# Optimization experiments

Hardware: AMD Instinct MI355X
Metric: run time of the kernel (lower is better)

Reference implementation:

```python
import jax, jax.numpy as jnp
import numpy as np

N, D, H, O, E = 4096, 1024, 4096, 1024, 8
TOP_K = 2

def setup_inputs() -> dict:
    key = jax.random.key(0)
    k = jax.random.split(key, 4)
    x  = jax.random.normal(k[0], (N, D), dtype=jnp.float32)
    Wg = jax.random.normal(k[1], (D, E), dtype=jnp.float32) * (1.0 / np.sqrt(D))
    W1 = jax.random.normal(k[2], (E, D, H), dtype=jnp.float32) * (1.0 / np.sqrt(D))
    b1 = jnp.zeros((E, H), dtype=jnp.float32)
    W2 = jax.random.normal(k[3], (E, H, O), dtype=jnp.float32) * (1.0 / np.sqrt(H))
    b2 = jnp.zeros((E, O), dtype=jnp.float32)
    return {"x": x, "Wg": Wg, "W1": W1, "b1": b1, "W2": W2, "b2": b2}

def reference(x, Wg, W1, b1, W2, b2):
    # Gate: Linear(bias=False) -> ReLU (lin() appends act) -> softmax
    logits = jax.nn.relu(x @ Wg)                      # [N, E]
    probs = jax.nn.softmax(logits, axis=1)            # [N, E]
    top_p, sel = jax.lax.top_k(probs, TOP_K)          # [N, K]
    top_p = top_p / jnp.sum(top_p, axis=-1, keepdims=True)
    # Per-token combine weights over experts: [N, E]
    combine = jnp.sum(jax.nn.one_hot(sel, E, dtype=x.dtype) * top_p[..., None], axis=1)
    # Experts: ReLU(x W1 + b1) -> ReLU(h W2 + b2); final ReLU because lin() adds act on output layer
    h = jax.nn.relu(jnp.einsum('nd,edh->enh', x, W1) + b1[:, None, :])   # [E, N, H]
    y = jax.nn.relu(jnp.einsum('enh,eho->eno', h, W2) + b2[:, None, :])  # [E, N, O]
    out = jnp.einsum('eno,ne->no', y, combine)                            # [N, O]
    return out
```

## Files before the change

### kernel.cpp

```cpp
#include <hip/hip_runtime.h>
#include <cstdint>

#define NTOK 4096
#define DDIM 1024
#define HDIM 4096
#define ODIM 1024
#define NEXP 8
#define NSLOT (2*NTOK)
#define MAXT128 72
#define MAXT256 40

typedef __bf16 bf16x8 __attribute__((ext_vector_type(8)));
typedef float  f32x4  __attribute__((ext_vector_type(4)));
typedef unsigned short ushort8v __attribute__((ext_vector_type(8)));

__device__ __forceinline__ unsigned short f2bf(float f) {
    union { float f; unsigned int u; } v; v.f = f;
    unsigned int r = (v.u + 0x7FFF + ((v.u >> 16) & 1)) >> 16;
    return (unsigned short)r;
}

typedef const void __attribute__((address_space(1)))* gas_ptr;
typedef void       __attribute__((address_space(3)))* las_ptr;

__global__ void gate_kernel(const float* __restrict__ x, const float* __restrict__ Wg,
                            int2* __restrict__ sel, float2* __restrict__ wts,
                            int* __restrict__ counts, unsigned short* __restrict__ xb) {
    int wave = threadIdx.x >> 6;
    int lane = threadIdx.x & 63;
    int n = blockIdx.x * 4 + wave;
    float acc[NEXP];
#pragma unroll
    for (int e = 0; e < NEXP; e++) acc[e] = 0.f;
    const float* xr = x + (size_t)n * DDIM;
    unsigned short* xbr = xb + (size_t)n * DDIM;
#pragma unroll
    for (int i = 0; i < 4; i++) {
        int d = i * 256 + lane * 4;
        float4 xv = *(const float4*)&xr[d];
        ushort4 o;
        o.x = f2bf(xv.x); o.y = f2bf(xv.y); o.z = f2bf(xv.z); o.w = f2bf(xv.w);
        *(ushort4*)&xbr[d] = o;
        const float* wr = Wg + (size_t)d * NEXP;
#pragma unroll
        for (int jj = 0; jj < 4; jj++) {
            float xs = (jj == 0) ? xv.x : (jj == 1) ? xv.y : (jj == 2) ? xv.z : xv.w;
#pragma unroll
            for (int e = 0; e < NEXP; e++)
                acc[e] = fmaf(xs, wr[jj * NEXP + e], acc[e]);
        }
    }
#pragma unroll
    for (int e = 0; e < NEXP; e++) {
#pragma unroll
        for (int off = 32; off >= 1; off >>= 1)
            acc[e] += __shfl_xor(acc[e], off, 64);
    }
    if (lane == 0) {
        float l0 = -1e30f, l1 = -1e30f; int e0 = 0, e1 = 0;
#pragma unroll
        for (int e = 0; e < NEXP; e++) {
            float v = fmaxf(acc[e], 0.f);
            if (v > l0)      { l1 = l0; e1 = e0; l0 = v; e0 = e; }
            else if (v > l1) { l1 = v;  e1 = e; }
        }
        float w0 = 1.f / (1.f + expf(l1 - l0));
        sel[n] = make_int2(e0, e1);
        wts[n] = make_float2(w0, 1.f - w0);
        atomicAdd(&counts[e0], 1);
        atomicAdd(&counts[e1], 1);
    }
}

__global__ void route_kernel(const int2* __restrict__ sel, const float2* __restrict__ wts,
                             const int* __restrict__ counts, int* __restrict__ offsets,
                             int4* __restrict__ t128, int* __restrict__ nt128,
                             int4* __restrict__ t256, int* __restrict__ nt256,
                             int* __restrict__ slot_token, float* __restrict__ slot_weight) {
    __shared__ int cur[NEXP];
    int t = threadIdx.x;
    if (t == 0) {
        int s = 0, n1 = 0, n2 = 0;
        for (int e = 0; e < NEXP; e++) {
            offsets[e] = s; cur[e] = s;
            int c = counts[e];
            for (int r = 0; r < c; r += 128)
                t128[n1++] = make_int4(e, s + r, min(128, c - r), 0);
            for (int r = 0; r < c; r += 256)
                t256[n2++] = make_int4(e, s + r, min(256, c - r), 0);
            s += c;
        }
        offsets[NEXP] = s;
        *nt128 = n1; *nt256 = n2;
    }
    __syncthreads();
    for (int n = t; n < NTOK; n += blockDim.x) {
        int2 se = sel[n]; float2 w = wts[n];
        int p0 = atomicAdd(&cur[se.x], 1);
        slot_token[p0] = n; slot_weight[p0] = w.x;
        int p1 = atomicAdd(&cur[se.y], 1);
        slot_token[p1] = n; slot_weight[p1] = w.y;
    }
}

__global__ void transpose_cast_kernel(const float* __restrict__ src, unsigned short* __restrict__ dst,
                                      int R, int C) {
    __shared__ float tile[64][65];
    int e = blockIdx.z;
    const float* s = src + (size_t)e * R * C;
    unsigned short* d = dst + (size_t)e * R * C;
    int t = threadIdx.x;
    int r0 = blockIdx.y * 64, c0 = blockIdx.x * 64;
#pragma unroll
    for (int p = 0; p < 4; p++) {
        int r = p * 16 + (t >> 4);
        int c = (t & 15) * 4;
        float4 v = *(const float4*)&s[(size_t)(r0 + r) * C + (c0 + c)];
        tile[r][c] = v.x; tile[r][c + 1] = v.y; tile[r][c + 2] = v.z; tile[r][c + 3] = v.w;
    }
    __syncthreads();
    int c = t >> 2, rb = (t & 3) * 16;
#pragma unroll
    for (int j = 0; j < 2; j++) {
        ushort8v v;
#pragma unroll
        for (int i = 0; i < 8; i++) v[i] = f2bf(tile[rb + j * 8 + i][c]);
        *(ushort8v*)&d[(size_t)(c0 + c) * R + (r0 + rb + j * 8)] = v;
    }
}

template <int MODE, int KDIM, int NDIM, int TN, int WN, int MINW, int NCOL>
__global__ __launch_bounds__(256, MINW) void moe_gemm_kernel(
    const unsigned short* __restrict__ A,
    const unsigned short* __restrict__ B,
    const float* __restrict__ bias,
    const int4* __restrict__ tile_meta,
    const int* __restrict__ ntiles,
    const int* __restrict__ slot_token,
    const float* __restrict__ slot_weight,
    unsigned short* __restrict__ h,
    float* __restrict__ out) {

    constexpr int WM = 4 / WN;
    constexpr int FM = 128 / WM / 16;
    constexpr int FN = TN / WN / 16;
    constexpr int NT = KDIM / 32;
    constexpr int LB = TN / 64;

    constexpr int nwg = NCOL * MAXT128;
    int bid = blockIdx.y * NCOL + blockIdx.x;
    int o = (bid & 7) * (nwg >> 3) + (bid >> 3);
    int tg = o / (8 * NCOL);
    int rem = o - tg * (8 * NCOL);
    int col = rem >> 3;
    int tile = tg * 8 + (rem & 7);
    if (tile >= *ntiles) return;
    int colBase = col * TN;

    int4 tm = tile_meta[tile];
    int e = tm.x, slotBase = tm.y, rows = tm.z;

    __shared__ __align__(16) unsigned short As[3][128 * 32];
    __shared__ __align__(16) unsigned short Bs[3][TN * 32];

    int tid = threadIdx.x;
    int w = tid >> 6, lane = tid & 63;
    int quad = lane >> 4, lr = lane & 15;
    int wm = w / WN, wn = w % WN;

    const unsigned short* Be = B + (size_t)e * NDIM * KDIM;

    int srow = tid >> 2;
    int g = (tid & 3) ^ ((tid >> 3) & 3);
    unsigned int aoff[2];
    unsigned int boff[LB];
#pragma unroll
    for (int i = 0; i < 2; i++) {
        int r = srow + i * 64;
        int slot = min(slotBase + r, NSLOT - 1);
        if constexpr (MODE == 1) aoff[i] = (unsigned)(slot_token[slot] * KDIM + g * 8);
        else                     aoff[i] = (unsigned)(slot * KDIM + g * 8);
    }
#pragma unroll
    for (int i = 0; i < LB; i++)
        boff[i] = (unsigned)((colBase + srow + i * 64) * KDIM + g * 8);

    auto stage = [&](int t, int sbuf) {
        char* Ab = (char*)&As[sbuf][0] + (size_t)(w * 64) * 16;
        char* Bb = (char*)&Bs[sbuf][0] + (size_t)(w * 64) * 16;
#pragma unroll
        for (int i = 0; i < 2; i++)
            __builtin_amdgcn_global_load_lds((gas_ptr)(A + aoff[i] + t * 32),
                                             (las_ptr)(Ab + i * 4096), 16, 0, 0);
#pragma unroll
        for (int i = 0; i < LB; i++)
            __builtin_amdgcn_global_load_lds((gas_ptr)(Be + boff[i] + t * 32),
                                             (las_ptr)(Bb + i * 4096), 16, 0, 0);
    };

    auto ldfrag = [&](const unsigned short* base, int R) -> bf16x8 {
        int s = quad ^ ((R >> 1) & 3);
        return *(const bf16x8*)((const char*)base + R * 64 + s * 16);
    };

    f32x4 zero = {0.f, 0.f, 0.f, 0.f};
    f32x4 acc[FM][FN];
#pragma unroll
    for (int m = 0; m < FM; m++)
#pragma unroll
        for (int n = 0; n < FN; n++) acc[m][n] = zero;

    stage(0, 0);
    stage(1, 1);
    int sb = 2, rb = 0;
    for (int t = 0; t < NT; ++t) {
        if (t + 2 < NT) {
            stage(t + 2, sb);
            if constexpr (LB == 4) asm volatile("s_waitcnt vmcnt(12)" ::: "memory");
            else                   asm volatile("s_waitcnt vmcnt(8)" ::: "memory");
        } else if (t + 1 < NT) {
            if constexpr (LB == 4) asm volatile("s_waitcnt vmcnt(6)" ::: "memory");
            else                   asm volatile("s_waitcnt vmcnt(4)" ::: "memory");
        } else {
            asm volatile("s_waitcnt vmcnt(0)" ::: "memory");
        }
        __builtin_amdgcn_s_barrier();

        bf16x8 af[FM], bf[FN];
        const unsigned short* Ar = As[rb];
        const unsigned short* Br = Bs[rb];
#pragma unroll
        for (int m = 0; m < FM; m++) af[m] = ldfrag(Ar, wm * (128 / WM) + m * 16 + lr);
#pragma unroll
        for (int n = 0; n < FN; n++) bf[n] = ldfrag(Br, wn * (TN / WN) + n * 16 + lr);
        asm volatile("s_waitcnt lgkmcnt(0)" ::: "memory");
        __builtin_amdgcn_s_barrier();

        __builtin_amdgcn_s_setprio(1);
#pragma unroll
        for (int m = 0; m < FM; m++)
#pragma unroll
            for (int n = 0; n < FN; n++)
                acc[m][n] = __builtin_amdgcn_mfma_f32_16x16x32_bf16(af[m], bf[n], acc[m][n], 0, 0, 0);
        __builtin_amdgcn_s_setprio(0);

        sb = (sb == 2) ? 0 : sb + 1;
        rb = (rb == 2) ? 0 : rb + 1;
    }

    if constexpr (MODE == 1) {
        const float* bv = bias + e * NDIM;
#pragma unroll
        for (int n = 0; n < FN; n++) {
            int gc = colBase + wn * (TN / WN) + n * 16 + lr;
            float bb = bv[gc];
#pragma unroll
            for (int m = 0; m < FM; m++) {
                int rl = wm * (128 / WM) + m * 16 + quad * 4;
#pragma unroll
                for (int i = 0; i < 4; i++) {
                    int r = rl + i;
                    if (r < rows) {
                        float v = fmaxf(acc[m][n][i] + bb, 0.f);
                        h[(size_t)(slotBase + r) * NDIM + gc] = f2bf(v);
                    }
                }
            }
        }
    } else {
        const float* bv = bias + e * NDIM;
#pragma unroll
        for (int m = 0; m < FM; m++) {
            int rl = wm * (128 / WM) + m * 16 + quad * 4;
#pragma unroll
            for (int i = 0; i < 4; i++) {
                int r = rl + i;
                if (r >= rows) continue;
                int s = slotBase + r;
                int tok = slot_token[s];
                float wgt = slot_weight[s];
                float* orow = out + (size_t)tok * ODIM;
#pragma unroll
                for (int n = 0; n < FN; n++) {
                    int gc = colBase + wn * (TN / WN) + n * 16 + lr;
                    float v = fmaxf(acc[m][n][i] + bv[gc], 0.f) * wgt;
                    atomicAdd(&orow[gc], v);
                }
            }
        }
    }
}

extern "C" void kernel_launch(void* const* d_in, const int* in_sizes, int n_in,
                              void* d_out, int out_size, void* d_ws, size_t ws_size,
                              hipStream_t stream) {
    const float* x  = (const float*)d_in[0];
    const float* Wg = (const float*)d_in[1];
    const float* W1 = (const float*)d_in[2];
    const float* b1 = (const float*)d_in[3];
    const float* W2 = (const float*)d_in[4];
    const float* b2 = (const float*)d_in[5];
    float* out = (float*)d_out;

    char* ws = (char*)d_ws;
    int*    counts      = (int*)(ws + 0);
    int*    offsets     = (int*)(ws + 64);
    int*    nt128       = (int*)(ws + 128);
    int*    nt256       = (int*)(ws + 132);
    int4*   t128        = (int4*)(ws + 256);
    int4*   t256        = (int4*)(ws + 2048);
    int2*   sel         = (int2*)(ws + 4096);
    float2* wts         = (float2*)(ws + 36864);
    int*    slot_token  = (int*)(ws + 69632);
    float*  slot_weight = (float*)(ws + 102400);
    unsigned short* xb  = (unsigned short*)(ws + 2097152);
    unsigned short* W1T = (unsigned short*)(ws + 10485760);
    unsigned short* W2T = (unsigned short*)(ws + 77594624);
    unsigned short* hbf = (unsigned short*)(ws + 144703488);

    hipMemsetAsync(d_out, 0, (size_t)NTOK * ODIM * sizeof(float), stream);
    hipMemsetAsync(ws, 0, 256, stream);

    gate_kernel<<<NTOK / 4, 256, 0, stream>>>(x, Wg, sel, wts, counts, xb);
    route_kernel<<<1, 512, 0, stream>>>(sel, wts, counts, offsets, t128, nt128, t256, nt256,
                                        slot_token, slot_weight);

    transpose_cast_kernel<<<dim3(HDIM / 64, DDIM / 64, NEXP), 256, 0, stream>>>(W1, W1T, DDIM, HDIM);
    transpose_cast_kernel<<<dim3(ODIM / 64, HDIM / 64, NEXP), 256, 0, stream>>>(W2, W2T, HDIM, ODIM);

    moe_gemm_kernel<1, DDIM, HDIM, 256, 4, 2, 16><<<dim3(16, MAXT128), 256, 0, stream>>>(
        xb, W1T, b1, t128, nt128, slot_token, slot_weight, hbf, nullptr);
    moe_gemm_kernel<2, HDIM, ODIM, 128, 2, 3, 8><<<dim3(8, MAXT128), 256, 0, stream>>>(
        hbf, W2T, b2, t128, nt128, slot_token, slot_weight, nullptr, out);
}
```

Before: 723.5 us.

## Software-pipeline MFMA loop, widen GEMM1 blocks, replace atomic scatter with combine kernel

The GEMM main loop is restructured to double-buffer register fragments, so LDS reads for the next K-step overlap the MFMAs of the current one. The MFMA operand order is swapped so the epilogue can write contiguous 4-wide vectors. The first GEMM now runs with 512 threads per block in a 2x4 wave layout, and its bf16 stores to h are vectorised. The second GEMM no longer does atomic scatter-adds into the output; it writes per-slot fp32 rows into reused workspace, and a new combine kernel forms the weighted sum of each token's two expert rows. This drops the output memset and atomic contention, but adds an extra pass that writes and reads the intermediate buffer.

```diff
diff --git a/kernel.cpp b/kernel.cpp
--- a/kernel.cpp
+++ b/kernel.cpp
@@ -8,7 +8,6 @@
 #define NEXP 8
 #define NSLOT (2*NTOK)
 #define MAXT128 72
-#define MAXT256 40
 
 typedef __bf16 bf16x8 __attribute__((ext_vector_type(8)));
 typedef float  f32x4  __attribute__((ext_vector_type(4)));
@@ -22,6 +21,13 @@
 
 typedef const void __attribute__((address_space(1)))* gas_ptr;
 typedef void       __attribute__((address_space(3)))* las_ptr;
+
+template <int N> __device__ __forceinline__ void vm_wait() {
+    if constexpr (N == 0) asm volatile("s_waitcnt vmcnt(0)" ::: "memory");
+    else if constexpr (N == 3) asm volatile("s_waitcnt vmcnt(3)" ::: "memory");
+    else if constexpr (N == 4) asm volatile("s_waitcnt vmcnt(4)" ::: "memory");
+    else if constexpr (N == 6) asm volatile("s_waitcnt vmcnt(6)" ::: "memory");
+}
 
 __global__ void gate_kernel(const float* __restrict__ x, const float* __restrict__ Wg,
                             int2* __restrict__ sel, float2* __restrict__ wts,
@@ -75,23 +81,21 @@
 __global__ void route_kernel(const int2* __restrict__ sel, const float2* __restrict__ wts,
                              const int* __restrict__ counts, int* __restrict__ offsets,
                              int4* __restrict__ t128, int* __restrict__ nt128,
-                             int4* __restrict__ t256, int* __restrict__ nt256,
-                             int* __restrict__ slot_token, float* __restrict__ slot_weight) {
+                             int* __restrict__ slot_token, float* __restrict__ slot_weight,
+                             int2* __restrict__ tokslot) {
     __shared__ int cur[NEXP];
     int t = threadIdx.x;
     if (t == 0) {
-        int s = 0, n1 = 0, n2 = 0;
+        int s = 0, n1 = 0;
         for (int e = 0; e < NEXP; e++) {
             offsets[e] = s; cur[e] = s;
             int c = counts[e];
             for (int r = 0; r < c; r += 128)
                 t128[n1++] = make_int4(e, s + r, min(128, c - r), 0);
-            for (int r = 0; r < c; r += 256)
-                t256[n2++] = make_int4(e, s + r, min(256, c - r), 0);
             s += c;
         }
         offsets[NEXP] = s;
-        *nt128 = n1; *nt256 = n2;
+        *nt128 = n1;
     }
     __syncthreads();
     for (int n = t; n < NTOK; n += blockDim.x) {
@@ -100,6 +104,7 @@
         slot_token[p0] = n; slot_weight[p0] = w.x;
         int p1 = atomicAdd(&cur[se.y], 1);
         slot_token[p1] = n; slot_weight[p1] = w.y;
+        tokslot[n] = make_int2(p0, p1);
     }
 }
 
@@ -129,23 +134,24 @@
     }
 }
 
-template <int MODE, int KDIM, int NDIM, int TN, int WN, int MINW, int NCOL>
-__global__ __launch_bounds__(256, MINW) void moe_gemm_kernel(
+template <int MODE, int KDIM, int NDIM, int THREADS, int TN, int WM, int WN, int MINW, int NCOL>
+__global__ __launch_bounds__(THREADS, MINW) void moe_gemm_kernel(
     const unsigned short* __restrict__ A,
     const unsigned short* __restrict__ B,
     const float* __restrict__ bias,
     const int4* __restrict__ tile_meta,
     const int* __restrict__ ntiles,
     const int* __restrict__ slot_token,
-    const float* __restrict__ slot_weight,
     unsigned short* __restrict__ h,
-    float* __restrict__ out) {
-
-    constexpr int WM = 4 / WN;
-    constexpr int FM = 128 / WM / 16;
-    constexpr int FN = TN / WN / 16;
+    float* __restrict__ yout) {
+
+    constexpr int TM = 128;
+    constexpr int RM = TM / WM, RN = TN / WN;
+    constexpr int FM = RM / 16, FN = RN / 16;
     constexpr int NT = KDIM / 32;
-    constexpr int LB = TN / 64;
+    constexpr int LA = TM * 4 / THREADS;
+    constexpr int LB = TN * 4 / THREADS;
+    constexpr int L  = LA + LB;
 
     constexpr int nwg = NCOL * MAXT128;
     int bid = blockIdx.y * NCOL + blockIdx.x;
@@ -160,7 +166,7 @@
     int4 tm = tile_meta[tile];
     int e = tm.x, slotBase = tm.y, rows = tm.z;
 
-    __shared__ __align__(16) unsigned short As[3][128 * 32];
+    __shared__ __align__(16) unsigned short As[3][TM * 32];
     __shared__ __align__(16) unsigned short Bs[3][TN * 32];
 
     int tid = threadIdx.x;
@@ -170,37 +176,51 @@
 
     const unsigned short* Be = B + (size_t)e * NDIM * KDIM;
 
-    int srow = tid >> 2;
-    int g = (tid & 3) ^ ((tid >> 3) & 3);
-    unsigned int aoff[2];
+    unsigned int aoff[LA];
     unsigned int boff[LB];
 #pragma unroll
-    for (int i = 0; i < 2; i++) {
-        int r = srow + i * 64;
+    for (int i = 0; i < LA; i++) {
+        int u = i * THREADS + tid;
+        int r = u >> 2, g = (u & 3) ^ ((u >> 3) & 3);
         int slot = min(slotBase + r, NSLOT - 1);
         if constexpr (MODE == 1) aoff[i] = (unsigned)(slot_token[slot] * KDIM + g * 8);
         else                     aoff[i] = (unsigned)(slot * KDIM + g * 8);
     }
 #pragma unroll
-    for (int i = 0; i < LB; i++)
-        boff[i] = (unsigned)((colBase + srow + i * 64) * KDIM + g * 8);
+    for (int i = 0; i < LB; i++) {
+        int u = i * THREADS + tid;
+        int r = u >> 2, g = (u & 3) ^ ((u >> 3) & 3);
+        boff[i] = (unsigned)((colBase + r) * KDIM + g * 8);
+    }
 
     auto stage = [&](int t, int sbuf) {
-        char* Ab = (char*)&As[sbuf][0] + (size_t)(w * 64) * 16;
-        char* Bb = (char*)&Bs[sbuf][0] + (size_t)(w * 64) * 16;
-#pragma unroll
-        for (int i = 0; i < 2; i++)
+        char* Ab = (char*)&As[sbuf][0] + w * 1024;
+        char* Bb = (char*)&Bs[sbuf][0] + w * 1024;
+#pragma unroll
+        for (int i = 0; i < LA; i++)
             __builtin_amdgcn_global_load_lds((gas_ptr)(A + aoff[i] + t * 32),
-                                             (las_ptr)(Ab + i * 4096), 16, 0, 0);
+                                             (las_ptr)(Ab + i * THREADS * 16), 16, 0, 0);
 #pragma unroll
         for (int i = 0; i < LB; i++)
             __builtin_amdgcn_global_load_lds((gas_ptr)(Be + boff[i] + t * 32),
-                                             (las_ptr)(Bb + i * 4096), 16, 0, 0);
+                                             (las_ptr)(Bb + i * THREADS * 16), 16, 0, 0);
     };
 
-    auto ldfrag = [&](const unsigned short* base, int R) -> bf16x8 {
-        int s = quad ^ ((R >> 1) & 3);
-        return *(const bf16x8*)((const char*)base + R * 64 + s * 16);
+    auto rdfrags = [&](bf16x8 (&af)[FM], bf16x8 (&bf)[FN], int buf) {
+        const char* Ar = (const char*)&As[buf][0];
+        const char* Br = (const char*)&Bs[buf][0];
+#pragma unroll
+        for (int m = 0; m < FM; m++) {
+            int R = wm * RM + m * 16 + lr;
+            int s = quad ^ ((R >> 1) & 3);
+            af[m] = *(const bf16x8*)(Ar + R * 64 + s * 16);
+        }
+#pragma unroll
+        for (int n = 0; n < FN; n++) {
+            int R = wn * RN + n * 16 + lr;
+            int s = quad ^ ((R >> 1) & 3);
+            bf[n] = *(const bf16x8*)(Br + R * 64 + s * 16);
+        }
     };
 
     f32x4 zero = {0.f, 0.f, 0.f, 0.f};
@@ -210,85 +230,109 @@
 #pragma unroll
         for (int n = 0; n < FN; n++) acc[m][n] = zero;
 
+    auto mfma_all = [&](bf16x8 (&af)[FM], bf16x8 (&bf)[FN]) {
+        __builtin_amdgcn_s_setprio(1);
+#pragma unroll
+        for (int m = 0; m < FM; m++)
+#pragma unroll
+            for (int n = 0; n < FN; n++)
+                acc[m][n] = __builtin_amdgcn_mfma_f32_16x16x32_bf16(bf[n], af[m], acc[m][n], 0, 0, 0);
+        __builtin_amdgcn_s_setprio(0);
+    };
+
+    bf16x8 afA[FM], bfA[FN], afB[FM], bfB[FN];
+
     stage(0, 0);
     stage(1, 1);
-    int sb = 2, rb = 0;
-    for (int t = 0; t < NT; ++t) {
-        if (t + 2 < NT) {
-            stage(t + 2, sb);
-            if constexpr (LB == 4) asm volatile("s_waitcnt vmcnt(12)" ::: "memory");
-            else                   asm volatile("s_waitcnt vmcnt(8)" ::: "memory");
-        } else if (t + 1 < NT) {
-            if constexpr (LB == 4) asm volatile("s_waitcnt vmcnt(6)" ::: "memory");
-            else                   asm volatile("s_waitcnt vmcnt(4)" ::: "memory");
-        } else {
-            asm volatile("s_waitcnt vmcnt(0)" ::: "memory");
-        }
+    vm_wait<L>();
+    __builtin_amdgcn_s_barrier();
+    rdfrags(afA, bfA, 0);
+    asm volatile("s_waitcnt lgkmcnt(0)" ::: "memory");
+    __builtin_amdgcn_sched_barrier(0);
+
+    int sb = 2, rb = 1;
+    for (int t = 0; t < NT; t += 2) {
+        bool st2 = (t + 2 < NT);
+        if (st2) stage(t + 2, sb);
+        if (st2) vm_wait<L>(); else vm_wait<0>();
         __builtin_amdgcn_s_barrier();
-
-        bf16x8 af[FM], bf[FN];
-        const unsigned short* Ar = As[rb];
-        const unsigned short* Br = Bs[rb];
-#pragma unroll
-        for (int m = 0; m < FM; m++) af[m] = ldfrag(Ar, wm * (128 / WM) + m * 16 + lr);
-#pragma unroll
-        for (int n = 0; n < FN; n++) bf[n] = ldfrag(Br, wn * (TN / WN) + n * 16 + lr);
+        rdfrags(afB, bfB, rb);
+        mfma_all(afA, bfA);
         asm volatile("s_waitcnt lgkmcnt(0)" ::: "memory");
+        __builtin_amdgcn_sched_barrier(0);
         __builtin_amdgcn_s_barrier();
-
-        __builtin_amdgcn_s_setprio(1);
-#pragma unroll
-        for (int m = 0; m < FM; m++)
-#pragma unroll
-            for (int n = 0; n < FN; n++)
-                acc[m][n] = __builtin_amdgcn_mfma_f32_16x16x32_bf16(af[m], bf[n], acc[m][n], 0, 0, 0);
-        __builtin_amdgcn_s_setprio(0);
-
         sb = (sb == 2) ? 0 : sb + 1;
         rb = (rb == 2) ? 0 : rb + 1;
-    }
-
+
+        bool st3 = (t + 3 < NT);
+        if (st3) stage(t + 3, sb);
+        if (st2) { if (st3) vm_wait<L>(); else vm_wait<0>(); }
+        __builtin_amdgcn_s_barrier();
+        if (st2) rdfrags(afA, bfA, rb);
+        mfma_all(afB, bfB);
+        asm volatile("s_waitcnt lgkmcnt(0)" ::: "memory");
+        __builtin_amdgcn_sched_barrier(0);
+        __builtin_amdgcn_s_barrier();
+        sb = (sb == 2) ? 0 : sb + 1;
+        rb = (rb == 2) ? 0 : rb + 1;
+    }
+
+    const float* bv = bias + e * NDIM;
     if constexpr (MODE == 1) {
-        const float* bv = bias + e * NDIM;
-#pragma unroll
-        for (int n = 0; n < FN; n++) {
-            int gc = colBase + wn * (TN / WN) + n * 16 + lr;
-            float bb = bv[gc];
-#pragma unroll
-            for (int m = 0; m < FM; m++) {
-                int rl = wm * (128 / WM) + m * 16 + quad * 4;
-#pragma unroll
-                for (int i = 0; i < 4; i++) {
-                    int r = rl + i;
-                    if (r < rows) {
-                        float v = fmaxf(acc[m][n][i] + bb, 0.f);
-                        h[(size_t)(slotBase + r) * NDIM + gc] = f2bf(v);
-                    }
+#pragma unroll
+        for (int m = 0; m < FM; m++) {
+            int r = wm * RM + m * 16 + lr;
+            if (r < rows) {
+                unsigned short* hrow = h + (size_t)(slotBase + r) * NDIM;
+#pragma unroll
+                for (int n = 0; n < FN; n++) {
+                    int c = colBase + wn * RN + n * 16 + quad * 4;
+                    float4 bb = *(const float4*)&bv[c];
+                    unsigned int lo = (unsigned)f2bf(fmaxf(acc[m][n][0] + bb.x, 0.f)) |
+                                      ((unsigned)f2bf(fmaxf(acc[m][n][1] + bb.y, 0.f)) << 16);
+                    unsigned int hi = (unsigned)f2bf(fmaxf(acc[m][n][2] + bb.z, 0.f)) |
+                                      ((unsigned)f2bf(fmaxf(acc[m][n][3] + bb.w, 0.f)) << 16);
+                    uint2 pv = make_uint2(lo, hi);
+                    *(uint2*)&hrow[c] = pv;
                 }
             }
         }
     } else {
-        const float* bv = bias + e * NDIM;
 #pragma unroll
         for (int m = 0; m < FM; m++) {
-            int rl = wm * (128 / WM) + m * 16 + quad * 4;
-#pragma unroll
-            for (int i = 0; i < 4; i++) {
-                int r = rl + i;
-                if (r >= rows) continue;
-                int s = slotBase + r;
-                int tok = slot_token[s];
-                float wgt = slot_weight[s];
-                float* orow = out + (size_t)tok * ODIM;
+            int r = wm * RM + m * 16 + lr;
+            if (r < rows) {
+                float* yrow = yout + (size_t)(slotBase + r) * NDIM;
 #pragma unroll
                 for (int n = 0; n < FN; n++) {
-                    int gc = colBase + wn * (TN / WN) + n * 16 + lr;
-                    float v = fmaxf(acc[m][n][i] + bv[gc], 0.f) * wgt;
-                    atomicAdd(&orow[gc], v);
+                    int c = colBase + wn * RN + n * 16 + quad * 4;
+                    float4 bb = *(const float4*)&bv[c];
+                    float4 v;
+                    v.x = fmaxf(acc[m][n][0] + bb.x, 0.f);
+                    v.y = fmaxf(acc[m][n][1] + bb.y, 0.f);
+                    v.z = fmaxf(acc[m][n][2] + bb.z, 0.f);
+                    v.w = fmaxf(acc[m][n][3] + bb.w, 0.f);
+                    *(float4*)&yrow[c] = v;
                 }
             }
         }
     }
+}
+
+__global__ void combine_kernel(const float* __restrict__ y, const int2* __restrict__ tokslot,
+                               const float2* __restrict__ wts, float* __restrict__ out) {
+    int n = blockIdx.x;
+    int t = threadIdx.x;
+    int2 ts = tokslot[n];
+    float2 w = wts[n];
+    float4 a = *(const float4*)&y[(size_t)ts.x * ODIM + t * 4];
+    float4 b = *(const float4*)&y[(size_t)ts.y * ODIM + t * 4];
+    float4 o;
+    o.x = w.x * a.x + w.y * b.x;
+    o.y = w.x * a.y + w.y * b.y;
+    o.z = w.x * a.z + w.y * b.z;
+    o.w = w.x * a.w + w.y * b.w;
+    *(float4*)&out[(size_t)n * ODIM + t * 4] = o;
 }
 
 extern "C" void kernel_launch(void* const* d_in, const int* in_sizes, int n_in,
@@ -306,30 +350,31 @@
     int*    counts      = (int*)(ws + 0);
     int*    offsets     = (int*)(ws + 64);
     int*    nt128       = (int*)(ws + 128);
-    int*    nt256       = (int*)(ws + 132);
     int4*   t128        = (int4*)(ws + 256);
-    int4*   t256        = (int4*)(ws + 2048);
     int2*   sel         = (int2*)(ws + 4096);
     float2* wts         = (float2*)(ws + 36864);
     int*    slot_token  = (int*)(ws + 69632);
     float*  slot_weight = (float*)(ws + 102400);
+    int2*   tokslot     = (int2*)(ws + 135168);
     unsigned short* xb  = (unsigned short*)(ws + 2097152);
     unsigned short* W1T = (unsigned short*)(ws + 10485760);
     unsigned short* W2T = (unsigned short*)(ws + 77594624);
     unsigned short* hbf = (unsigned short*)(ws + 144703488);
-
-    hipMemsetAsync(d_out, 0, (size_t)NTOK * ODIM * sizeof(float), stream);
+    float* ybf = (float*)(ws + 10485760);
+
     hipMemsetAsync(ws, 0, 256, stream);
 
     gate_kernel<<<NTOK / 4, 256, 0, stream>>>(x, Wg, sel, wts, counts, xb);
-    route_kernel<<<1, 512, 0, stream>>>(sel, wts, counts, offsets, t128, nt128, t256, nt256,
-                                        slot_token, slot_weight);
+    route_kernel<<<1, 512, 0, stream>>>(sel, wts, counts, offsets, t128, nt128,
+                                        slot_token, slot_weight, tokslot);
 
     transpose_cast_kernel<<<dim3(HDIM / 64, DDIM / 64, NEXP), 256, 0, stream>>>(W1, W1T, DDIM, HDIM);
     transpose_cast_kernel<<<dim3(ODIM / 64, HDIM / 64, NEXP), 256, 0, stream>>>(W2, W2T, HDIM, ODIM);
 
-    moe_gemm_kernel<1, DDIM, HDIM, 256, 4, 2, 16><<<dim3(16, MAXT128), 256, 0, stream>>>(
-        xb, W1T, b1, t128, nt128, slot_token, slot_weight, hbf, nullptr);
-    moe_gemm_kernel<2, HDIM, ODIM, 128, 2, 3, 8><<<dim3(8, MAXT128), 256, 0, stream>>>(
-        hbf, W2T, b2, t128, nt128, slot_token, slot_weight, nullptr, out);
-}
+    moe_gemm_kernel<1, DDIM, HDIM, 512, 256, 2, 4, 2, 16><<<dim3(16, MAXT128), 512, 0, stream>>>(
+        xb, W1T, b1, t128, nt128, slot_token, hbf, nullptr);
+    moe_gemm_kernel<2, HDIM, ODIM, 256, 128, 2, 2, 2, 8><<<dim3(8, MAXT128), 256, 0, stream>>>(
+        hbf, W2T, b2, t128, nt128, slot_token, nullptr, ybf);
+
+    combine_kernel<<<NTOK, 256, 0, stream>>>(ybf, tokslot, wts, out);
+}
```

New measurement: 715.7 us. No clear change (-1.1%).
